# Kernel tuning notes

Hardware: AMD Instinct MI355X
Metric: run time of the kernel (lower is better)

Reference implementation:

```python
import jax, jax.numpy as jnp
import numpy as np

H = 1024      # hidden_size
V = 50257     # output_size (vocab)
L = 100       # max_length


def setup_inputs() -> dict:
    key = jax.random.key(0)
    ks = jax.random.split(key, 14)
    s = 0.02
    return {
        "token": jax.random.randint(ks[0], (1,), 0, V),
        "hidden": jax.random.normal(ks[1], (1, 1, H), jnp.float32),
        "encoder_outputs": jax.random.normal(ks[2], (L, H), jnp.float32),
        "embedding": jax.random.normal(ks[3], (V, H), jnp.float32) * s,
        "attn_w": jax.random.normal(ks[4], (L, 2 * H), jnp.float32) * s,
        "attn_b": jnp.zeros((L,), jnp.float32),
        "comb_w": jax.random.normal(ks[5], (H, 2 * H), jnp.float32) * s,
        "comb_b": jnp.zeros((H,), jnp.float32),
        "w_ih": jax.random.normal(ks[6], (3 * H, H), jnp.float32) * s,
        "w_hh": jax.random.normal(ks[7], (3 * H, H), jnp.float32) * s,
        "b_ih": jnp.zeros((3 * H,), jnp.float32),
        "b_hh": jnp.zeros((3 * H,), jnp.float32),
        "out_w": jax.random.normal(ks[8], (V, H), jnp.float32) * s,
        "out_b": jnp.zeros((V,), jnp.float32),
    }


def reference(token, hidden, encoder_outputs, embedding, attn_w, attn_b,
              comb_w, comb_b, w_ih, w_hh, b_ih, b_hh, out_w, out_b):
    # embedding lookup; dropout is identity in eval mode
    emb = embedding[token]                                   # [1, H]
    h0 = hidden[0]                                           # [1, H]
    # attention over encoder positions
    attn_in = jnp.concatenate([emb, h0], axis=1)             # [1, 2H]
    attn_weights = jax.nn.softmax(attn_in @ attn_w.T + attn_b, axis=1)  # [1, L]
    attn_applied = attn_weights @ encoder_outputs            # [1, H]
    # combine + relu
    x = jnp.concatenate([emb, attn_applied], axis=1) @ comb_w.T + comb_b  # [1, H]
    x = jax.nn.relu(x)
    # single GRU cell step (PyTorch gate order: r, z, n)
    gi = x @ w_ih.T + b_ih                                   # [1, 3H]
    gh = h0 @ w_hh.T + b_hh                                  # [1, 3H]
    ir, iz, in_ = jnp.split(gi, 3, axis=1)
    hr, hz, hn = jnp.split(gh, 3, axis=1)
    r = jax.nn.sigmoid(ir + hr)
    z = jax.nn.sigmoid(iz + hz)
    n = jnp.tanh(in_ + r * hn)
    h_new = (1.0 - z) * n + z * h0                           # [1, H]
    # output projection + log_softmax
    output = jax.nn.log_softmax(h_new @ out_w.T + out_b, axis=1)  # [1, V]
    return output, h_new[None], attn_weights
```

## Files before the change

kernel.cpp:

```cpp
#include <hip/hip_runtime.h>
#include <hip/hip_bf16.h>

#define H 1024
#define V 50257
#define L 100
#define NPART 1024


__global__ void kA_logits(const int* token, const float* hidden, const float* embedding,
                          const float* attn_w, const float* attn_b, float* ws_log) {
    int lane = threadIdx.x;
    int r = blockIdx.x;
    const float4* e4 = (const float4*)(embedding + (size_t)token[0] * H);
    const float4* h4 = (const float4*)hidden;
    const float4* wr = (const float4*)(attn_w + (size_t)r * (2 * H));
    float acc = 0.f;
    #pragma unroll
    for (int j = 0; j < 4; j++) {
        float4 w = wr[lane + 64 * j];
        float4 v = e4[lane + 64 * j];
        acc += w.x * v.x + w.y * v.y + w.z * v.z + w.w * v.w;
    }
    #pragma unroll
    for (int j = 0; j < 4; j++) {
        float4 w = wr[256 + lane + 64 * j];
        float4 v = h4[lane + 64 * j];
        acc += w.x * v.x + w.y * v.y + w.z * v.z + w.w * v.w;
    }
    #pragma unroll
    for (int off = 32; off > 0; off >>= 1) acc += __shfl_down(acc, off, 64);
    if (lane == 0) ws_log[r] = acc + attn_b[r];
}


__global__ void kS_softmax_apply(const float* ws_log, const float* enc,
                                 float* ws_app, float* out_attnw) {
    __shared__ float red[8];
    __shared__ float aw_s[128];
    __shared__ float part[4][64];
    int t = threadIdx.x, lane = t & 63, wv = t >> 6;

    float x = (t < L) ? ws_log[t] : -1e30f;
    float mv = x;
    #pragma unroll
    for (int off = 32; off > 0; off >>= 1) mv = fmaxf(mv, __shfl_down(mv, off, 64));
    if (lane == 0) red[wv] = mv;
    __syncthreads();
    float m = fmaxf(fmaxf(red[0], red[1]), fmaxf(red[2], red[3]));
    float e = (t < L) ? expf(x - m) : 0.f;
    float sv = e;
    #pragma unroll
    for (int off = 32; off > 0; off >>= 1) sv += __shfl_down(sv, off, 64);
    if (lane == 0) red[4 + wv] = sv;
    __syncthreads();
    float s = red[4] + red[5] + red[6] + red[7];
    float aw = e / s;
    if (t < 128) aw_s[t] = aw;
    if (blockIdx.x == 0 && t < L) out_attnw[t] = aw;
    __syncthreads();

    int h = blockIdx.x * 64 + lane;
    float acc = 0.f;
    #pragma unroll
    for (int i = 0; i < 25; i++) {
        int l = wv * 25 + i;
        acc += aw_s[l] * enc[l * H + h];
    }
    part[wv][lane] = acc;
    __syncthreads();
    if (wv == 0)
        ws_app[h] = part[0][lane] + part[1][lane] + part[2][lane] + part[3][lane];
}


__global__ void kComb(const int* token, const float* embedding, const float* ws_app,
                      const float* comb_w, const float* comb_b, float* ws_x) {
    int lane = threadIdx.x & 63, wv = threadIdx.x >> 6;
    int r = blockIdx.x * 4 + wv;
    const float4* e4 = (const float4*)(embedding + (size_t)token[0] * H);
    const float4* a4 = (const float4*)ws_app;
    const float4* wr = (const float4*)(comb_w + (size_t)r * (2 * H));
    float acc = 0.f;
    #pragma unroll
    for (int j = 0; j < 4; j++) {
        float4 w = wr[lane + 64 * j];
        float4 v = e4[lane + 64 * j];
        acc += w.x * v.x + w.y * v.y + w.z * v.z + w.w * v.w;
    }
    #pragma unroll
    for (int j = 0; j < 4; j++) {
        float4 w = wr[256 + lane + 64 * j];
        float4 v = a4[lane + 64 * j];
        acc += w.x * v.x + w.y * v.y + w.z * v.z + w.w * v.w;
    }
    #pragma unroll
    for (int off = 32; off > 0; off >>= 1) acc += __shfl_down(acc, off, 64);
    if (lane == 0) ws_x[r] = fmaxf(acc + comb_b[r], 0.0f);
}


__global__ void kC_gru(const float* ws_x, const float* hidden,
                       const float* w_ih, const float* w_hh,
                       const float* b_ih, const float* b_hh,
                       float* out_h, float* ws_hn) {
    int lane = threadIdx.x & 63, wv = threadIdx.x >> 6;
    int h = blockIdx.x * 4 + wv;
    const float4* x4 = (const float4*)ws_x;
    const float4* h4 = (const float4*)hidden;
    float acc[6] = {0.f, 0.f, 0.f, 0.f, 0.f, 0.f};
    #pragma unroll
    for (int j = 0; j < 4; j++) {
        float4 xv = x4[lane + 64 * j];
        float4 hv = h4[lane + 64 * j];
        #pragma unroll
        for (int k = 0; k < 3; k++) {
            float4 w = ((const float4*)(w_ih + (size_t)(k * H + h) * H))[lane + 64 * j];
            acc[k] += w.x * xv.x + w.y * xv.y + w.z * xv.z + w.w * xv.w;
        }
        #pragma unroll
        for (int k = 0; k < 3; k++) {
            float4 w = ((const float4*)(w_hh + (size_t)(k * H + h) * H))[lane + 64 * j];
            acc[3 + k] += w.x * hv.x + w.y * hv.y + w.z * hv.z + w.w * hv.w;
        }
    }
    #pragma unroll
    for (int off = 32; off > 0; off >>= 1) {
        #pragma unroll
        for (int k = 0; k < 6; k++) acc[k] += __shfl_down(acc[k], off, 64);
    }
    if (lane == 0) {
        float ir = acc[0] + b_ih[h], iz = acc[1] + b_ih[H + h], in_ = acc[2] + b_ih[2 * H + h];
        float hr = acc[3] + b_hh[h], hz = acc[4] + b_hh[H + h], hn = acc[5] + b_hh[2 * H + h];
        float r = 1.f / (1.f + expf(-(ir + hr)));
        float z = 1.f / (1.f + expf(-(iz + hz)));
        float n = tanhf(in_ + r * hn);
        float h0 = hidden[h];
        float v = (1.f - z) * n + z * h0;
        out_h[h] = v;
        ws_hn[h] = v;
    }
}


__global__ void kD_outproj(const float* hn, const float* out_w, const float* out_b,
                           float* out_logits, float* ws_pm, float* ws_ps) {
    __shared__ float sm[4], ss[4];
    int lane = threadIdx.x & 63;
    int wv   = threadIdx.x >> 6;
    const float4* h4 = (const float4*)hn;
    float4 h0 = h4[lane], h1 = h4[lane + 64], h2 = h4[lane + 128], h3 = h4[lane + 192];
    float m = -1e30f, s = 0.f;
    int wid = blockIdx.x * 4 + wv;
    for (int r0 = wid * 4; r0 < V; r0 += NPART * 16) {
        float acc[4] = {0.f, 0.f, 0.f, 0.f};
        #pragma unroll
        for (int i = 0; i < 4; i++) {
            int r = r0 + i;
            if (r < V) {
                const float4* wr = (const float4*)(out_w + (size_t)r * H);
                float4 a = wr[lane], b = wr[lane + 64], c = wr[lane + 128], d = wr[lane + 192];
                acc[i] = a.x * h0.x + a.y * h0.y + a.z * h0.z + a.w * h0.w
                       + b.x * h1.x + b.y * h1.y + b.z * h1.z + b.w * h1.w
                       + c.x * h2.x + c.y * h2.y + c.z * h2.z + c.w * h2.w
                       + d.x * h3.x + d.y * h3.y + d.z * h3.z + d.w * h3.w;
            }
        }
        #pragma unroll
        for (int off = 32; off > 0; off >>= 1) {
            #pragma unroll
            for (int i = 0; i < 4; i++) acc[i] += __shfl_down(acc[i], off, 64);
        }
        if (lane == 0) {
            #pragma unroll
            for (int i = 0; i < 4; i++) {
                int r = r0 + i;
                if (r < V) {
                    float lg = acc[i] + out_b[r];
                    out_logits[r] = lg;
                    float nm = fmaxf(m, lg);
                    s = s * expf(m - nm) + expf(lg - nm);
                    m = nm;
                }
            }
        }
    }
    if (lane == 0) { sm[wv] = m; ss[wv] = s; }
    __syncthreads();
    if (threadIdx.x == 0) {
        m = sm[0]; s = ss[0];
        #pragma unroll
        for (int i = 1; i < 4; i++) {
            float nm = fmaxf(m, sm[i]);
            s = s * expf(m - nm) + ss[i] * expf(sm[i] - nm);
            m = nm;
        }
        ws_pm[blockIdx.x] = m;
        ws_ps[blockIdx.x] = s;
    }
}


__global__ void kE_finalize(const float* ws_pm, const float* ws_ps, float* out) {
    __shared__ float sm[4], ss[4], fm, fs;
    int t = threadIdx.x;
    float m = -1e30f, s = 0.f;
    for (int i = t; i < NPART; i += 256) {
        float pm = ws_pm[i], ps = ws_ps[i];
        float nm = fmaxf(m, pm);
        s = s * expf(m - nm) + ps * expf(pm - nm);
        m = nm;
    }
    #pragma unroll
    for (int off = 32; off > 0; off >>= 1) {
        float om = __shfl_down(m, off, 64);
        float os = __shfl_down(s, off, 64);
        float nm = fmaxf(m, om);
        s = s * expf(m - nm) + os * expf(om - nm);
        m = nm;
    }
    int lane = t & 63, wv = t >> 6;
    if (lane == 0) { sm[wv] = m; ss[wv] = s; }
    __syncthreads();
    if (t == 0) {
        m = sm[0]; s = ss[0];
        #pragma unroll
        for (int i = 1; i < 4; i++) {
            float nm = fmaxf(m, sm[i]);
            s = s * expf(m - nm) + ss[i] * expf(sm[i] - nm);
            m = nm;
        }
        fm = m; fs = logf(s);
    }
    __syncthreads();
    float M = fm, LS = fs;
    for (int v = blockIdx.x * 256 + t; v < V; v += gridDim.x * 256)
        out[v] = out[v] - M - LS;
}


extern "C" void kernel_launch(void* const* d_in, const int* in_sizes, int n_in,
                              void* d_out, int out_size, void* d_ws, size_t ws_size,
                              hipStream_t stream) {
    const int*   token     = (const int*)d_in[0];
    const float* hidden    = (const float*)d_in[1];
    const float* enc       = (const float*)d_in[2];
    const float* embedding = (const float*)d_in[3];
    const float* attn_w    = (const float*)d_in[4];
    const float* attn_b    = (const float*)d_in[5];
    const float* comb_w    = (const float*)d_in[6];
    const float* comb_b    = (const float*)d_in[7];
    const float* w_ih      = (const float*)d_in[8];
    const float* w_hh      = (const float*)d_in[9];
    const float* b_ih      = (const float*)d_in[10];
    const float* b_hh      = (const float*)d_in[11];
    const float* out_w     = (const float*)d_in[12];
    const float* out_b     = (const float*)d_in[13];

    float* out = (float*)d_out;
    float* ws  = (float*)d_ws;
    float* ws_log = ws;
    float* ws_app = ws + 128;
    float* ws_x   = ws + 1152;
    float* ws_pm  = ws + 2176;
    float* ws_ps  = ws + 3200;
    float* ws_hn  = ws + 4224;

    kA_logits<<<dim3(L), dim3(64), 0, stream>>>(token, hidden, embedding,
                                                attn_w, attn_b, ws_log);
    kS_softmax_apply<<<dim3(16), dim3(256), 0, stream>>>(ws_log, enc, ws_app, out + V + H);
    kComb<<<dim3(256), dim3(256), 0, stream>>>(token, embedding, ws_app,
                                               comb_w, comb_b, ws_x);
    kC_gru<<<dim3(256), dim3(256), 0, stream>>>(ws_x, hidden, w_ih, w_hh, b_ih, b_hh,
                                                out + V, ws_hn);
    kD_outproj<<<dim3(NPART), dim3(256), 0, stream>>>(ws_hn, out_w, out_b, out, ws_pm, ws_ps);
    kE_finalize<<<dim3(128), dim3(256), 0, stream>>>(ws_pm, ws_ps, out);
}
```

Baseline: 58.39 us.

## Fuse attention logits, softmax, apply and combine into one redundant-compute kernel

Merges the attention-logit, softmax/apply and combine kernels into a single kernel launched on 128 blocks. Each block recomputes all 100 attention logits, the softmax and the full attention-applied vector, then computes its own 8 rows of the combine layer. This removes two kernel launches and their global round-trips, at the cost of every block redundantly reading attn_w (about 800KB) and encoder_outputs (about 400KB), which mostly hit in cache.

```diff
diff --git a/kernel.cpp b/kernel.cpp
--- a/kernel.cpp
+++ b/kernel.cpp
@@ -7,40 +7,47 @@
 #define NPART 1024
 
 
-__global__ void kA_logits(const int* token, const float* hidden, const float* embedding,
-                          const float* attn_w, const float* attn_b, float* ws_log) {
-    int lane = threadIdx.x;
-    int r = blockIdx.x;
+__device__ __forceinline__ float wave_sum(float v) {
+    #pragma unroll
+    for (int off = 32; off > 0; off >>= 1) v += __shfl_down(v, off, 64);
+    return v;
+}
+
+__device__ __forceinline__ float dot1024(const float4* w, const float4* x, int lane) {
+    float acc = 0.f;
+    #pragma unroll
+    for (int j = 0; j < 4; j++) {
+        float4 a = w[lane + 64 * j];
+        float4 b = x[lane + 64 * j];
+        acc += a.x * b.x + a.y * b.y + a.z * b.z + a.w * b.w;
+    }
+    return acc;
+}
+
+
+__global__ void kSC(const int* token, const float* hidden, const float* embedding,
+                    const float* attn_w, const float* attn_b, const float* enc,
+                    const float* comb_w, const float* comb_b,
+                    float* ws_x, float* out_attnw) {
+    __shared__ float lg[L];
+    __shared__ float aw[128];
+    __shared__ float4 app4[256];
+    __shared__ float red[8];
+    int t = threadIdx.x, lane = t & 63, wv = t >> 6;
+
     const float4* e4 = (const float4*)(embedding + (size_t)token[0] * H);
     const float4* h4 = (const float4*)hidden;
-    const float4* wr = (const float4*)(attn_w + (size_t)r * (2 * H));
-    float acc = 0.f;
-    #pragma unroll
-    for (int j = 0; j < 4; j++) {
-        float4 w = wr[lane + 64 * j];
-        float4 v = e4[lane + 64 * j];
-        acc += w.x * v.x + w.y * v.y + w.z * v.z + w.w * v.w;
-    }
-    #pragma unroll
-    for (int j = 0; j < 4; j++) {
-        float4 w = wr[256 + lane + 64 * j];
-        float4 v = h4[lane + 64 * j];
-        acc += w.x * v.x + w.y * v.y + w.z * v.z + w.w * v.w;
-    }
-    #pragma unroll
-    for (int off = 32; off > 0; off >>= 1) acc += __shfl_down(acc, off, 64);
-    if (lane == 0) ws_log[r] = acc + attn_b[r];
-}
-
-
-__global__ void kS_softmax_apply(const float* ws_log, const float* enc,
-                                 float* ws_app, float* out_attnw) {
-    __shared__ float red[8];
-    __shared__ float aw_s[128];
-    __shared__ float part[4][64];
-    int t = threadIdx.x, lane = t & 63, wv = t >> 6;
-
-    float x = (t < L) ? ws_log[t] : -1e30f;
+
+    for (int i = 0; i < 25; i++) {
+        int r = wv * 25 + i;
+        const float4* wr = (const float4*)(attn_w + (size_t)r * (2 * H));
+        float acc = dot1024(wr, e4, lane) + dot1024(wr + 256, h4, lane);
+        acc = wave_sum(acc);
+        if (lane == 0) lg[r] = acc + attn_b[r];
+    }
+    __syncthreads();
+
+    float x = (t < L) ? lg[t] : -1e30f;
     float mv = x;
     #pragma unroll
     for (int off = 32; off > 0; off >>= 1) mv = fmaxf(mv, __shfl_down(mv, off, 64));
@@ -48,61 +55,42 @@
     __syncthreads();
     float m = fmaxf(fmaxf(red[0], red[1]), fmaxf(red[2], red[3]));
     float e = (t < L) ? expf(x - m) : 0.f;
-    float sv = e;
-    #pragma unroll
-    for (int off = 32; off > 0; off >>= 1) sv += __shfl_down(sv, off, 64);
+    float sv = wave_sum(e);
     if (lane == 0) red[4 + wv] = sv;
     __syncthreads();
     float s = red[4] + red[5] + red[6] + red[7];
-    float aw = e / s;
-    if (t < 128) aw_s[t] = aw;
-    if (blockIdx.x == 0 && t < L) out_attnw[t] = aw;
-    __syncthreads();
-
-    int h = blockIdx.x * 64 + lane;
-    float acc = 0.f;
-    #pragma unroll
-    for (int i = 0; i < 25; i++) {
-        int l = wv * 25 + i;
-        acc += aw_s[l] * enc[l * H + h];
-    }
-    part[wv][lane] = acc;
-    __syncthreads();
-    if (wv == 0)
-        ws_app[h] = part[0][lane] + part[1][lane] + part[2][lane] + part[3][lane];
-}
-
-
-__global__ void kComb(const int* token, const float* embedding, const float* ws_app,
-                      const float* comb_w, const float* comb_b, float* ws_x) {
-    int lane = threadIdx.x & 63, wv = threadIdx.x >> 6;
-    int r = blockIdx.x * 4 + wv;
-    const float4* e4 = (const float4*)(embedding + (size_t)token[0] * H);
-    const float4* a4 = (const float4*)ws_app;
-    const float4* wr = (const float4*)(comb_w + (size_t)r * (2 * H));
-    float acc = 0.f;
-    #pragma unroll
-    for (int j = 0; j < 4; j++) {
-        float4 w = wr[lane + 64 * j];
-        float4 v = e4[lane + 64 * j];
-        acc += w.x * v.x + w.y * v.y + w.z * v.z + w.w * v.w;
-    }
-    #pragma unroll
-    for (int j = 0; j < 4; j++) {
-        float4 w = wr[256 + lane + 64 * j];
-        float4 v = a4[lane + 64 * j];
-        acc += w.x * v.x + w.y * v.y + w.z * v.z + w.w * v.w;
-    }
-    #pragma unroll
-    for (int off = 32; off > 0; off >>= 1) acc += __shfl_down(acc, off, 64);
-    if (lane == 0) ws_x[r] = fmaxf(acc + comb_b[r], 0.0f);
-}
-
-
-__global__ void kC_gru(const float* ws_x, const float* hidden,
-                       const float* w_ih, const float* w_hh,
-                       const float* b_ih, const float* b_hh,
-                       float* out_h, float* ws_hn) {
+    if (t < 128) aw[t] = e / s;
+    if (blockIdx.x == 0 && t < L) out_attnw[t] = e / s;
+    __syncthreads();
+
+    {
+        int c = wv * 64 + lane;
+        float4 acc4 = make_float4(0.f, 0.f, 0.f, 0.f);
+        for (int l = 0; l < L; l++) {
+            float a = aw[l];
+            float4 ev = ((const float4*)(enc + (size_t)l * H))[c];
+            acc4.x += a * ev.x; acc4.y += a * ev.y;
+            acc4.z += a * ev.z; acc4.w += a * ev.w;
+        }
+        app4[c] = acc4;
+    }
+    __syncthreads();
+
+    #pragma unroll
+    for (int k = 0; k < 2; k++) {
+        int r = (blockIdx.x * 4 + wv) * 2 + k;
+        const float4* wr = (const float4*)(comb_w + (size_t)r * (2 * H));
+        float acc = dot1024(wr, e4, lane) + dot1024(wr + 256, app4, lane);
+        acc = wave_sum(acc);
+        if (lane == 0) ws_x[r] = fmaxf(acc + comb_b[r], 0.0f);
+    }
+}
+
+
+__global__ void kGRU(const float* ws_x, const float* hidden,
+                     const float* w_ih, const float* w_hh,
+                     const float* b_ih, const float* b_hh,
+                     float* out_h, float* ws_hn) {
     int lane = threadIdx.x & 63, wv = threadIdx.x >> 6;
     int h = blockIdx.x * 4 + wv;
     const float4* x4 = (const float4*)ws_x;
@@ -258,20 +246,15 @@
 
     float* out = (float*)d_out;
     float* ws  = (float*)d_ws;
-    float* ws_log = ws;
-    float* ws_app = ws + 128;
-    float* ws_x   = ws + 1152;
-    float* ws_pm  = ws + 2176;
-    float* ws_ps  = ws + 3200;
-    float* ws_hn  = ws + 4224;
-
-    kA_logits<<<dim3(L), dim3(64), 0, stream>>>(token, hidden, embedding,
-                                                attn_w, attn_b, ws_log);
-    kS_softmax_apply<<<dim3(16), dim3(256), 0, stream>>>(ws_log, enc, ws_app, out + V + H);
-    kComb<<<dim3(256), dim3(256), 0, stream>>>(token, embedding, ws_app,
-                                               comb_w, comb_b, ws_x);
-    kC_gru<<<dim3(256), dim3(256), 0, stream>>>(ws_x, hidden, w_ih, w_hh, b_ih, b_hh,
-                                                out + V, ws_hn);
+    float* ws_x   = ws;
+    float* ws_pm  = ws + 1024;
+    float* ws_ps  = ws + 2048;
+    float* ws_hn  = ws + 3072;
+
+    kSC<<<dim3(128), dim3(256), 0, stream>>>(token, hidden, embedding, attn_w, attn_b,
+                                             enc, comb_w, comb_b, ws_x, out + V + H);
+    kGRU<<<dim3(256), dim3(256), 0, stream>>>(ws_x, hidden, w_ih, w_hh, b_ih, b_hh,
+                                              out + V, ws_hn);
     kD_outproj<<<dim3(NPART), dim3(256), 0, stream>>>(ws_hn, out_w, out_b, out, ws_pm, ws_ps);
     kE_finalize<<<dim3(128), dim3(256), 0, stream>>>(ws_pm, ws_ps, out);
 }
```

Measured after the change: 78.15 us. 33.8% more time.
